# Performance work log

Hardware: AMD Instinct MI355X
Metric: run time of the kernel (lower is better)

The kernel has to match this reference:

```python
import jax, jax.numpy as jnp
import numpy as np

B, T, I, H, C = 4096, 512, 3, 32, 3  # batch, seq_len, input, hidden, classes


def setup_inputs() -> dict:
    key = jax.random.key(0)
    ks = jax.random.split(key, 7)
    s = 1.0 / np.sqrt(H)  # PyTorch LSTM init scale
    return {
        "x": jax.random.normal(ks[0], (B, T, I), dtype=jnp.float32),
        "W_ih": jax.random.normal(ks[1], (4 * H, I), dtype=jnp.float32) * s,
        "W_hh": jax.random.normal(ks[2], (4 * H, H), dtype=jnp.float32) * s,
        "b_ih": jax.random.normal(ks[3], (4 * H,), dtype=jnp.float32) * s,
        "b_hh": jax.random.normal(ks[4], (4 * H,), dtype=jnp.float32) * s,
        "W_fc": jax.random.normal(ks[5], (C, H), dtype=jnp.float32) * s,
        "b_fc": jax.random.normal(ks[6], (C,), dtype=jnp.float32) * s,
    }


def reference(x, W_ih, W_hh, b_ih, b_hh, W_fc, b_fc):
    # Precompute input contribution to all gates for every timestep: (B,T,4H)
    xg = jnp.einsum("bti,gi->btg", x, W_ih) + b_ih + b_hh
    h0 = jnp.zeros((x.shape[0], H), dtype=x.dtype)
    c0 = jnp.zeros_like(h0)

    def step(carry, xt):
        h, c = carry
        g = xt + h @ W_hh.T  # (B,4H)
        i_g, f_g, g_g, o_g = jnp.split(g, 4, axis=-1)  # PyTorch gate order i,f,g,o
        i_g = jax.nn.sigmoid(i_g)
        f_g = jax.nn.sigmoid(f_g)
        g_g = jnp.tanh(g_g)
        o_g = jax.nn.sigmoid(o_g)
        c = f_g * c + i_g * g_g
        h = o_g * jnp.tanh(c)
        return (h, c), None

    (h_last, _), _ = jax.lax.scan(step, (h0, c0), jnp.swapaxes(xg, 0, 1))
    return h_last @ W_fc.T + b_fc  # (B, num_classes)
```

## Files before the change

kernel.cpp:

```cpp
#include <hip/hip_runtime.h>
#include <cstdint>

#define B_TOT 4096
#define T_LEN 512
#define CHUNK 256
#define LOG2E 1.44269504088896340736f
#define HSTR  40

typedef _Float16 f16x8 __attribute__((ext_vector_type(8)));
typedef _Float16 f16x4 __attribute__((ext_vector_type(4)));
typedef float    f32x4 __attribute__((ext_vector_type(4)));

__device__ __forceinline__ float ex2(float v)  { return __builtin_amdgcn_exp2f(v); }
__device__ __forceinline__ float rcp_(float v) { return __builtin_amdgcn_rcpf(v); }

__global__ __launch_bounds__(256, 2)
void lstm_pr(const float* __restrict__ x,
             const float* __restrict__ W_ih,
             const float* __restrict__ W_hh,
             const float* __restrict__ b_ih,
             const float* __restrict__ b_hh,
             const float* __restrict__ W_fc,
             const float* __restrict__ b_fc,
             float* __restrict__ out)
{
    __shared__ __align__(16) _Float16 hbuf[2][8][HSTR];
    __shared__ __align__(16) _Float16 xbuf[CHUNK / 2][8][8];

    const int tid  = threadIdx.x;
    const int wave = tid >> 6;
    const int lane = tid & 63;
    const int n    = lane & 15;
    const int kq   = lane >> 4;
    const int nb   = n & 7;
    const int tb   = blockIdx.x * 8;

    const int   gate_m = n & 3;
    const int   hl_m   = n >> 2;
    const int   R1     = gate_m * 32 + 8 * wave + hl_m;
    const int   R2     = R1 + 4;
    const float sm     = (gate_m == 2) ? (-2.0f * LOG2E) : (-LOG2E);

    f16x8 aW1, aW2;
#pragma unroll
    for (int j = 0; j < 8; ++j) {
        aW1[j] = (_Float16)(sm * W_hh[R1 * 32 + 8 * kq + j]);
        aW2[j] = (_Float16)(sm * W_hh[R2 * 32 + 8 * kq + j]);
    }
    f16x8 a21 = {}, a22 = {};
    if (kq == 0) {
        a21[0] = (_Float16)(sm * W_ih[R1 * 3 + 0]);
        a21[1] = (_Float16)(sm * W_ih[R1 * 3 + 1]);
        a21[2] = (_Float16)(sm * W_ih[R1 * 3 + 2]);
        a21[3] = (_Float16)(sm * (b_ih[R1] + b_hh[R1]));
        a22[0] = (_Float16)(sm * W_ih[R2 * 3 + 0]);
        a22[1] = (_Float16)(sm * W_ih[R2 * 3 + 1]);
        a22[2] = (_Float16)(sm * W_ih[R2 * 3 + 2]);
        a22[3] = (_Float16)(sm * (b_ih[R2] + b_hh[R2]));
    }

    const int hid_s = 8 * wave + kq + ((n >> 3) ? 4 : 0);

    if (tid < 160) ((int*)&hbuf[0][0][0])[tid] = 0;

    const float K2 = -2.0f * LOG2E;
    float c = 0.0f;
    const f32x4 z = {0.f, 0.f, 0.f, 0.f};
    f32x4 accx1, accx2;

    const bool hi = (n >> 3) != 0;

    for (int tc = 0; tc < T_LEN; tc += CHUNK) {
#pragma unroll
        for (int s = 0; s < 8; ++s) {
            const int idx = tid + s * 256;
            const int tl = idx >> 3, m = idx & 7;
            const float* xp = x + ((size_t)(tb + m) * T_LEN + (tc + tl)) * 3;
            f16x4 v;
            v[0] = (_Float16)xp[0]; v[1] = (_Float16)xp[1];
            v[2] = (_Float16)xp[2]; v[3] = (_Float16)1.0f;
            *(f16x4*)&xbuf[tl >> 1][m][4 * (tl & 1)] = v;
        }
        __syncthreads();

        f16x8 xp = *(const f16x8*)&xbuf[0][nb][0];
        {
            const f16x8 b2 = __builtin_shufflevector(xp, xp, 0, 1, 2, 3, 0, 1, 2, 3);
            accx1 = __builtin_amdgcn_mfma_f32_16x16x32_f16(a21, b2, z, 0, 0, 0);
            accx2 = __builtin_amdgcn_mfma_f32_16x16x32_f16(a22, b2, z, 0, 0, 0);
        }

        for (int t2 = 0; t2 < CHUNK / 2; ++t2) {
            {
                const f16x8 bh = *(const f16x8*)&hbuf[0][nb][8 * kq];
                const f32x4 ac1 = __builtin_amdgcn_mfma_f32_16x16x32_f16(aW1, bh, accx1, 0, 0, 0);
                const f32x4 ac2 = __builtin_amdgcn_mfma_f32_16x16x32_f16(aW2, bh, accx2, 0, 0, 0);

                const float a0 = hi ? ac2[0] : ac1[0];
                const float a1 = hi ? ac2[1] : ac1[1];
                const float a2 = hi ? ac2[2] : ac1[2];
                const float a3 = hi ? ac2[3] : ac1[3];

                const float ei = ex2(a0), ef = ex2(a1), eg = ex2(a2), eo = ex2(a3);
                const float pi = 1.0f + ei, pf = 1.0f + ef, pg = 1.0f + eg;
                const float mg = 1.0f - eg;
                const float pp = pi * pg, qn = mg * pf;
                c = fmaf(c, pp, qn) * rcp_(pf * pp);
                const float ec = ex2(c * K2);
                const float po = 1.0f + eo, pc = 1.0f + ec, mc = 1.0f - ec;
                const float h = mc * rcp_(po * pc);
                hbuf[1][nb][hid_s] = (_Float16)h;

                const f16x8 b2 = __builtin_shufflevector(xp, xp, 4, 5, 6, 7, 4, 5, 6, 7);
                accx1 = __builtin_amdgcn_mfma_f32_16x16x32_f16(a21, b2, z, 0, 0, 0);
                accx2 = __builtin_amdgcn_mfma_f32_16x16x32_f16(a22, b2, z, 0, 0, 0);
            }
            __syncthreads();

            {
                const f16x8 bh = *(const f16x8*)&hbuf[1][nb][8 * kq];
                const int t2n = (t2 + 1) & (CHUNK / 2 - 1);
                const f16x8 xpN = *(const f16x8*)&xbuf[t2n][nb][0];

                const f32x4 ac1 = __builtin_amdgcn_mfma_f32_16x16x32_f16(aW1, bh, accx1, 0, 0, 0);
                const f32x4 ac2 = __builtin_amdgcn_mfma_f32_16x16x32_f16(aW2, bh, accx2, 0, 0, 0);

                const float a0 = hi ? ac2[0] : ac1[0];
                const float a1 = hi ? ac2[1] : ac1[1];
                const float a2 = hi ? ac2[2] : ac1[2];
                const float a3 = hi ? ac2[3] : ac1[3];

                const float ei = ex2(a0), ef = ex2(a1), eg = ex2(a2), eo = ex2(a3);
                const float pi = 1.0f + ei, pf = 1.0f + ef, pg = 1.0f + eg;
                const float mg = 1.0f - eg;
                const float pp = pi * pg, qn = mg * pf;
                c = fmaf(c, pp, qn) * rcp_(pf * pp);
                const float ec = ex2(c * K2);
                const float po = 1.0f + eo, pc = 1.0f + ec, mc = 1.0f - ec;
                const float h = mc * rcp_(po * pc);
                hbuf[0][nb][hid_s] = (_Float16)h;

                const f16x8 b2 = __builtin_shufflevector(xpN, xpN, 0, 1, 2, 3, 0, 1, 2, 3);
                accx1 = __builtin_amdgcn_mfma_f32_16x16x32_f16(a21, b2, z, 0, 0, 0);
                accx2 = __builtin_amdgcn_mfma_f32_16x16x32_f16(a22, b2, z, 0, 0, 0);
                xp = xpN;
            }
            __syncthreads();
        }
    }

    if (tid < 24) {
        const int m = tid / 3, cc = tid % 3;
        float acc = b_fc[cc];
#pragma unroll
        for (int k = 0; k < 32; ++k)
            acc = fmaf(W_fc[cc * 32 + k], (float)hbuf[0][m][k], acc);
        out[(tb + m) * 3 + cc] = acc;
    }
}

extern "C" void kernel_launch(void* const* d_in, const int* in_sizes, int n_in,
                              void* d_out, int out_size, void* d_ws, size_t ws_size,
                              hipStream_t stream) {
    const float* x    = (const float*)d_in[0];
    const float* W_ih = (const float*)d_in[1];
    const float* W_hh = (const float*)d_in[2];
    const float* b_ih = (const float*)d_in[3];
    const float* b_hh = (const float*)d_in[4];
    const float* W_fc = (const float*)d_in[5];
    const float* b_fc = (const float*)d_in[6];
    float* out = (float*)d_out;

    dim3 grid(B_TOT / 8);
    dim3 block(256);
    lstm_pr<<<grid, block, 0, stream>>>(x, W_ih, W_hh, b_ih, b_hh, W_fc, b_fc, out);
}
```

Baseline: 184.6 us.

## Run each LSTM recurrence in a single wavefront with swizzle-based hidden-state exchange

Restructures the kernel so one 64-lane wavefront handles 4 sequences and all 128 gate rows using 8 MFMAs per step, instead of 4 waves splitting the gates for 8 sequences. The hidden state is exchanged between lanes with ds_swizzle rather than an LDS buffer guarded by __syncthreads each timestep, removing block barriers from the serial recurrence. The whole sequence's inputs are staged into LDS up front. In exchange each wave does roughly twice the MFMA work per sequence, holds many more weight registers, and the grid has 1024 single-wave blocks, which changes occupancy and latency hiding.

New measurement: 244.1 us. +32.2%, slower.

```diff
diff --git a/kernel.cpp b/kernel.cpp
--- a/kernel.cpp
+++ b/kernel.cpp
@@ -3,19 +3,19 @@
 
 #define B_TOT 4096
 #define T_LEN 512
-#define CHUNK 256
 #define LOG2E 1.44269504088896340736f
-#define HSTR  40
 
 typedef _Float16 f16x8 __attribute__((ext_vector_type(8)));
 typedef _Float16 f16x4 __attribute__((ext_vector_type(4)));
+typedef _Float16 f16x2 __attribute__((ext_vector_type(2)));
 typedef float    f32x4 __attribute__((ext_vector_type(4)));
+typedef unsigned int u32x4 __attribute__((ext_vector_type(4)));
 
 __device__ __forceinline__ float ex2(float v)  { return __builtin_amdgcn_exp2f(v); }
 __device__ __forceinline__ float rcp_(float v) { return __builtin_amdgcn_rcpf(v); }
 
-__global__ __launch_bounds__(256, 2)
-void lstm_pr(const float* __restrict__ x,
+__global__ __launch_bounds__(64, 1)
+void lstm_wv(const float* __restrict__ x,
              const float* __restrict__ W_ih,
              const float* __restrict__ W_hh,
              const float* __restrict__ b_ih,
@@ -24,138 +24,122 @@
              const float* __restrict__ b_fc,
              float* __restrict__ out)
 {
-    __shared__ __align__(16) _Float16 hbuf[2][8][HSTR];
-    __shared__ __align__(16) _Float16 xbuf[CHUNK / 2][8][8];
+    __shared__ __align__(16) _Float16 xbuf[T_LEN / 2][4][8];
+    __shared__ float hfin[4][32];
 
-    const int tid  = threadIdx.x;
-    const int wave = tid >> 6;
-    const int lane = tid & 63;
+    const int lane = threadIdx.x;
     const int n    = lane & 15;
     const int kq   = lane >> 4;
-    const int nb   = n & 7;
-    const int tb   = blockIdx.x * 8;
+    const int b    = n & 3;
+    const int d    = n >> 2;
+    const int gb0  = blockIdx.x << 2;
 
-    const int   gate_m = n & 3;
-    const int   hl_m   = n >> 2;
-    const int   R1     = gate_m * 32 + 8 * wave + hl_m;
-    const int   R2     = R1 + 4;
-    const float sm     = (gate_m == 2) ? (-2.0f * LOG2E) : (-LOG2E);
-
-    f16x8 aW1, aW2;
+    f16x8 aW[8], A2e[8], A2o[8];
 #pragma unroll
     for (int j = 0; j < 8; ++j) {
-        aW1[j] = (_Float16)(sm * W_hh[R1 * 32 + 8 * kq + j]);
-        aW2[j] = (_Float16)(sm * W_hh[R2 * 32 + 8 * kq + j]);
-    }
-    f16x8 a21 = {}, a22 = {};
-    if (kq == 0) {
-        a21[0] = (_Float16)(sm * W_ih[R1 * 3 + 0]);
-        a21[1] = (_Float16)(sm * W_ih[R1 * 3 + 1]);
-        a21[2] = (_Float16)(sm * W_ih[R1 * 3 + 2]);
-        a21[3] = (_Float16)(sm * (b_ih[R1] + b_hh[R1]));
-        a22[0] = (_Float16)(sm * W_ih[R2 * 3 + 0]);
-        a22[1] = (_Float16)(sm * W_ih[R2 * 3 + 1]);
-        a22[2] = (_Float16)(sm * W_ih[R2 * 3 + 2]);
-        a22[3] = (_Float16)(sm * (b_ih[R2] + b_hh[R2]));
+        const int   g   = j & 3;
+        const int   R   = 32 * g + 8 * d + 4 * (j >> 2) + b;
+        const float smj = (g == 2) ? (-2.0f * LOG2E) : (-LOG2E);
+#pragma unroll
+        for (int jj = 0; jj < 8; ++jj)
+            aW[j][jj] = (_Float16)(smj * W_hh[R * 32 + 8 * kq + jj]);
+        f16x8 e = {}, o = {};
+        if (kq == 0) {
+            const _Float16 w0 = (_Float16)(smj * W_ih[R * 3 + 0]);
+            const _Float16 w1 = (_Float16)(smj * W_ih[R * 3 + 1]);
+            const _Float16 w2 = (_Float16)(smj * W_ih[R * 3 + 2]);
+            const _Float16 wb = (_Float16)(smj * (b_ih[R] + b_hh[R]));
+            e[0] = w0; e[1] = w1; e[2] = w2; e[3] = wb;
+            o[4] = w0; o[5] = w1; o[6] = w2; o[7] = wb;
+        }
+        A2e[j] = e; A2o[j] = o;
     }
 
-    const int hid_s = 8 * wave + kq + ((n >> 3) ? 4 : 0);
+    for (int s = 0; s < 32; ++s) {
+        const int id = lane + (s << 6);
+        const int t = id >> 2, bb = id & 3;
+        const float* xg = x + ((size_t)(gb0 + bb) * T_LEN + t) * 3;
+        f16x4 v;
+        v[0] = (_Float16)xg[0]; v[1] = (_Float16)xg[1];
+        v[2] = (_Float16)xg[2]; v[3] = (_Float16)1.0f;
+        *(f16x4*)&xbuf[t >> 1][bb][(t & 1) << 2] = v;
+    }
+    __syncthreads();
 
-    if (tid < 160) ((int*)&hbuf[0][0][0])[tid] = 0;
+    const bool selj = (d >= 2);
+    const bool selr = (d & 1) != 0;
+    const f32x4 z = {0.f, 0.f, 0.f, 0.f};
 
-    const float K2 = -2.0f * LOG2E;
-    float c = 0.0f;
-    const f32x4 z = {0.f, 0.f, 0.f, 0.f};
-    f32x4 accx1, accx2;
+    u32x4 bhu = {0u, 0u, 0u, 0u};
+    float c0 = 0.f, c1 = 0.f;
+    float h0 = 0.f, h1 = 0.f;
 
-    const bool hi = (n >> 3) != 0;
+    f16x8 xp = *(const f16x8*)&xbuf[0][b][0];
 
-    for (int tc = 0; tc < T_LEN; tc += CHUNK) {
+    for (int t2 = 0; t2 < T_LEN / 2; ++t2) {
+        const f16x8 xpN = *(const f16x8*)&xbuf[(t2 + 1) & (T_LEN / 2 - 1)][b][0];
 #pragma unroll
-        for (int s = 0; s < 8; ++s) {
-            const int idx = tid + s * 256;
-            const int tl = idx >> 3, m = idx & 7;
-            const float* xp = x + ((size_t)(tb + m) * T_LEN + (tc + tl)) * 3;
-            f16x4 v;
-            v[0] = (_Float16)xp[0]; v[1] = (_Float16)xp[1];
-            v[2] = (_Float16)xp[2]; v[3] = (_Float16)1.0f;
-            *(f16x4*)&xbuf[tl >> 1][m][4 * (tl & 1)] = v;
+        for (int par = 0; par < 2; ++par) {
+            f32x4 acc[8];
+#pragma unroll
+            for (int j = 0; j < 8; ++j) {
+                const f32x4 ax = __builtin_amdgcn_mfma_f32_16x16x32_f16(
+                    par ? A2o[j] : A2e[j], xp, z, 0, 0, 0);
+                acc[j] = __builtin_amdgcn_mfma_f32_16x16x32_f16(
+                    aW[j], __builtin_bit_cast(f16x8, bhu), ax, 0, 0, 0);
+            }
+            float av[4][2];
+#pragma unroll
+            for (int g = 0; g < 4; ++g) {
+                const float v0 = selj ? acc[g + 4][0] : acc[g][0];
+                const float v1 = selj ? acc[g + 4][1] : acc[g][1];
+                const float v2 = selj ? acc[g + 4][2] : acc[g][2];
+                const float v3 = selj ? acc[g + 4][3] : acc[g][3];
+                av[g][0] = selr ? v2 : v0;
+                av[g][1] = selr ? v3 : v1;
+            }
+            {
+                const float ei = ex2(av[0][0]), ef = ex2(av[1][0]);
+                const float eg = ex2(av[2][0]), eo = ex2(av[3][0]);
+                const float pi = 1.f + ei, pf = 1.f + ef, pg = 1.f + eg;
+                const float mg = 1.f - eg;
+                const float pp = pi * pg, qn = mg * pf;
+                c0 = fmaf(c0, pp, qn) * rcp_(pf * pp);
+                const float ec = ex2(c0 * (-2.0f * LOG2E));
+                const float po = 1.f + eo, pc = 1.f + ec, mc = 1.f - ec;
+                h0 = mc * rcp_(po * pc);
+            }
+            {
+                const float ei = ex2(av[0][1]), ef = ex2(av[1][1]);
+                const float eg = ex2(av[2][1]), eo = ex2(av[3][1]);
+                const float pi = 1.f + ei, pf = 1.f + ef, pg = 1.f + eg;
+                const float mg = 1.f - eg;
+                const float pp = pi * pg, qn = mg * pf;
+                c1 = fmaf(c1, pp, qn) * rcp_(pf * pp);
+                const float ec = ex2(c1 * (-2.0f * LOG2E));
+                const float po = 1.f + eo, pc = 1.f + ec, mc = 1.f - ec;
+                h1 = mc * rcp_(po * pc);
+            }
+            f16x2 hp; hp[0] = (_Float16)h0; hp[1] = (_Float16)h1;
+            const int pk = __builtin_bit_cast(int, hp);
+            bhu[0] = (unsigned)__builtin_amdgcn_ds_swizzle(pk, 0x0013);
+            bhu[1] = (unsigned)__builtin_amdgcn_ds_swizzle(pk, 0x0093);
+            bhu[2] = (unsigned)__builtin_amdgcn_ds_swizzle(pk, 0x0113);
+            bhu[3] = (unsigned)__builtin_amdgcn_ds_swizzle(pk, 0x0193);
         }
-        __syncthreads();
-
-        f16x8 xp = *(const f16x8*)&xbuf[0][nb][0];
-        {
-            const f16x8 b2 = __builtin_shufflevector(xp, xp, 0, 1, 2, 3, 0, 1, 2, 3);
-            accx1 = __builtin_amdgcn_mfma_f32_16x16x32_f16(a21, b2, z, 0, 0, 0);
-            accx2 = __builtin_amdgcn_mfma_f32_16x16x32_f16(a22, b2, z, 0, 0, 0);
-        }
-
-        for (int t2 = 0; t2 < CHUNK / 2; ++t2) {
-            {
-                const f16x8 bh = *(const f16x8*)&hbuf[0][nb][8 * kq];
-                const f32x4 ac1 = __builtin_amdgcn_mfma_f32_16x16x32_f16(aW1, bh, accx1, 0, 0, 0);
-                const f32x4 ac2 = __builtin_amdgcn_mfma_f32_16x16x32_f16(aW2, bh, accx2, 0, 0, 0);
-
-                const float a0 = hi ? ac2[0] : ac1[0];
-                const float a1 = hi ? ac2[1] : ac1[1];
-                const float a2 = hi ? ac2[2] : ac1[2];
-                const float a3 = hi ? ac2[3] : ac1[3];
-
-                const float ei = ex2(a0), ef = ex2(a1), eg = ex2(a2), eo = ex2(a3);
-                const float pi = 1.0f + ei, pf = 1.0f + ef, pg = 1.0f + eg;
-                const float mg = 1.0f - eg;
-                const float pp = pi * pg, qn = mg * pf;
-                c = fmaf(c, pp, qn) * rcp_(pf * pp);
-                const float ec = ex2(c * K2);
-                const float po = 1.0f + eo, pc = 1.0f + ec, mc = 1.0f - ec;
-                const float h = mc * rcp_(po * pc);
-                hbuf[1][nb][hid_s] = (_Float16)h;
-
-                const f16x8 b2 = __builtin_shufflevector(xp, xp, 4, 5, 6, 7, 4, 5, 6, 7);
-                accx1 = __builtin_amdgcn_mfma_f32_16x16x32_f16(a21, b2, z, 0, 0, 0);
-                accx2 = __builtin_amdgcn_mfma_f32_16x16x32_f16(a22, b2, z, 0, 0, 0);
-            }
-            __syncthreads();
-
-            {
-                const f16x8 bh = *(const f16x8*)&hbuf[1][nb][8 * kq];
-                const int t2n = (t2 + 1) & (CHUNK / 2 - 1);
-                const f16x8 xpN = *(const f16x8*)&xbuf[t2n][nb][0];
-
-                const f32x4 ac1 = __builtin_amdgcn_mfma_f32_16x16x32_f16(aW1, bh, accx1, 0, 0, 0);
-                const f32x4 ac2 = __builtin_amdgcn_mfma_f32_16x16x32_f16(aW2, bh, accx2, 0, 0, 0);
-
-                const float a0 = hi ? ac2[0] : ac1[0];
-                const float a1 = hi ? ac2[1] : ac1[1];
-                const float a2 = hi ? ac2[2] : ac1[2];
-                const float a3 = hi ? ac2[3] : ac1[3];
-
-                const float ei = ex2(a0), ef = ex2(a1), eg = ex2(a2), eo = ex2(a3);
-                const float pi = 1.0f + ei, pf = 1.0f + ef, pg = 1.0f + eg;
-                const float mg = 1.0f - eg;
-                const float pp = pi * pg, qn = mg * pf;
-                c = fmaf(c, pp, qn) * rcp_(pf * pp);
-                const float ec = ex2(c * K2);
-                const float po = 1.0f + eo, pc = 1.0f + ec, mc = 1.0f - ec;
-                const float h = mc * rcp_(po * pc);
-                hbuf[0][nb][hid_s] = (_Float16)h;
-
-                const f16x8 b2 = __builtin_shufflevector(xpN, xpN, 0, 1, 2, 3, 0, 1, 2, 3);
-                accx1 = __builtin_amdgcn_mfma_f32_16x16x32_f16(a21, b2, z, 0, 0, 0);
-                accx2 = __builtin_amdgcn_mfma_f32_16x16x32_f16(a22, b2, z, 0, 0, 0);
-                xp = xpN;
-            }
-            __syncthreads();
-        }
+        xp = xpN;
     }
 
-    if (tid < 24) {
-        const int m = tid / 3, cc = tid % 3;
+    hfin[b][8 * kq + 2 * d + 0] = h0;
+    hfin[b][8 * kq + 2 * d + 1] = h1;
+    __syncthreads();
+    if (lane < 12) {
+        const int m = lane / 3, cc = lane - 3 * m;
         float acc = b_fc[cc];
 #pragma unroll
         for (int k = 0; k < 32; ++k)
-            acc = fmaf(W_fc[cc * 32 + k], (float)hbuf[0][m][k], acc);
-        out[(tb + m) * 3 + cc] = acc;
+            acc = fmaf(W_fc[cc * 32 + k], hfin[m][k], acc);
+        out[(gb0 + m) * 3 + cc] = acc;
     }
 }
 
@@ -171,7 +155,7 @@
     const float* b_fc = (const float*)d_in[6];
     float* out = (float*)d_out;
 
-    dim3 grid(B_TOT / 8);
-    dim3 block(256);
-    lstm_pr<<<grid, block, 0, stream>>>(x, W_ih, W_hh, b_ih, b_hh, W_fc, b_fc, out);
+    dim3 grid(B_TOT / 4);
+    dim3 block(64);
+    lstm_wv<<<grid, block, 0, stream>>>(x, W_ih, W_hh, b_ih, b_hh, W_fc, b_fc, out);
 }
```

## Interleave two independent batch tiles per block to hide recurrence latency

Applied to the files above, without the earlier changes.

Each block now processes 16 sequences as two independent 8-sequence groups (A and B) whose timesteps alternate. The hbuf buffers are repurposed so each group's h-state lives in its own slot, and the next group's h is prefetched into registers across the barrier. The aim is to overlap one group's MFMA and transcendental latency with the other's, keeping the serial chain per barrier shorter in effective cost. Blocks are halved in number, occupancy hint drops to 1, and CHUNK is halved to fit the larger x staging buffer. This risks fewer resident waves per CU and more barriers per real timestep.

Result: slower. 252.8 us (+36.9%).

```diff
diff --git a/kernel.cpp b/kernel.cpp
--- a/kernel.cpp
+++ b/kernel.cpp
@@ -3,7 +3,7 @@
 
 #define B_TOT 4096
 #define T_LEN 512
-#define CHUNK 256
+#define CHUNK 128
 #define LOG2E 1.44269504088896340736f
 #define HSTR  40
 
@@ -14,8 +14,8 @@
 __device__ __forceinline__ float ex2(float v)  { return __builtin_amdgcn_exp2f(v); }
 __device__ __forceinline__ float rcp_(float v) { return __builtin_amdgcn_rcpf(v); }
 
-__global__ __launch_bounds__(256, 2)
-void lstm_pr(const float* __restrict__ x,
+__global__ __launch_bounds__(256, 1)
+void lstm_2t(const float* __restrict__ x,
              const float* __restrict__ W_ih,
              const float* __restrict__ W_hh,
              const float* __restrict__ b_ih,
@@ -25,7 +25,7 @@
              float* __restrict__ out)
 {
     __shared__ __align__(16) _Float16 hbuf[2][8][HSTR];
-    __shared__ __align__(16) _Float16 xbuf[CHUNK / 2][8][8];
+    __shared__ __align__(16) _Float16 xbuf[CHUNK / 2][16][8];
 
     const int tid  = threadIdx.x;
     const int wave = tid >> 6;
@@ -33,7 +33,7 @@
     const int n    = lane & 15;
     const int kq   = lane >> 4;
     const int nb   = n & 7;
-    const int tb   = blockIdx.x * 8;
+    const int tb   = blockIdx.x * 16;
 
     const int   gate_m = n & 3;
     const int   hl_m   = n >> 2;
@@ -60,101 +60,143 @@
     }
 
     const int hid_s = 8 * wave + kq + ((n >> 3) ? 4 : 0);
-
-    if (tid < 160) ((int*)&hbuf[0][0][0])[tid] = 0;
+    const bool hi   = (n >> 3) != 0;
+
+    for (int i = tid; i < 320; i += 256) ((int*)&hbuf[0][0][0])[i] = 0;
 
     const float K2 = -2.0f * LOG2E;
-    float c = 0.0f;
+    float cA = 0.0f, cB = 0.0f;
     const f32x4 z = {0.f, 0.f, 0.f, 0.f};
-    f32x4 accx1, accx2;
-
-    const bool hi = (n >> 3) != 0;
+    f32x4 accA1, accA2, accB1, accB2;
+    f16x8 bhA = {}, bhB = {};
 
     for (int tc = 0; tc < T_LEN; tc += CHUNK) {
 #pragma unroll
         for (int s = 0; s < 8; ++s) {
             const int idx = tid + s * 256;
-            const int tl = idx >> 3, m = idx & 7;
-            const float* xp = x + ((size_t)(tb + m) * T_LEN + (tc + tl)) * 3;
+            const int tl = idx >> 4, m = idx & 15;
+            const float* xp_ = x + ((size_t)(tb + m) * T_LEN + (tc + tl)) * 3;
             f16x4 v;
-            v[0] = (_Float16)xp[0]; v[1] = (_Float16)xp[1];
-            v[2] = (_Float16)xp[2]; v[3] = (_Float16)1.0f;
+            v[0] = (_Float16)xp_[0]; v[1] = (_Float16)xp_[1];
+            v[2] = (_Float16)xp_[2]; v[3] = (_Float16)1.0f;
             *(f16x4*)&xbuf[tl >> 1][m][4 * (tl & 1)] = v;
         }
         __syncthreads();
 
-        f16x8 xp = *(const f16x8*)&xbuf[0][nb][0];
+        f16x8 xpA = *(const f16x8*)&xbuf[0][nb][0];
+        f16x8 xpB = *(const f16x8*)&xbuf[0][8 + nb][0];
         {
-            const f16x8 b2 = __builtin_shufflevector(xp, xp, 0, 1, 2, 3, 0, 1, 2, 3);
-            accx1 = __builtin_amdgcn_mfma_f32_16x16x32_f16(a21, b2, z, 0, 0, 0);
-            accx2 = __builtin_amdgcn_mfma_f32_16x16x32_f16(a22, b2, z, 0, 0, 0);
+            const f16x8 bA = __builtin_shufflevector(xpA, xpA, 0, 1, 2, 3, 0, 1, 2, 3);
+            accA1 = __builtin_amdgcn_mfma_f32_16x16x32_f16(a21, bA, z, 0, 0, 0);
+            accA2 = __builtin_amdgcn_mfma_f32_16x16x32_f16(a22, bA, z, 0, 0, 0);
+            const f16x8 bB = __builtin_shufflevector(xpB, xpB, 0, 1, 2, 3, 0, 1, 2, 3);
+            accB1 = __builtin_amdgcn_mfma_f32_16x16x32_f16(a21, bB, z, 0, 0, 0);
+            accB2 = __builtin_amdgcn_mfma_f32_16x16x32_f16(a22, bB, z, 0, 0, 0);
         }
 
         for (int t2 = 0; t2 < CHUNK / 2; ++t2) {
-            {
-                const f16x8 bh = *(const f16x8*)&hbuf[0][nb][8 * kq];
-                const f32x4 ac1 = __builtin_amdgcn_mfma_f32_16x16x32_f16(aW1, bh, accx1, 0, 0, 0);
-                const f32x4 ac2 = __builtin_amdgcn_mfma_f32_16x16x32_f16(aW2, bh, accx2, 0, 0, 0);
-
-                const float a0 = hi ? ac2[0] : ac1[0];
-                const float a1 = hi ? ac2[1] : ac1[1];
-                const float a2 = hi ? ac2[2] : ac1[2];
-                const float a3 = hi ? ac2[3] : ac1[3];
-
-                const float ei = ex2(a0), ef = ex2(a1), eg = ex2(a2), eo = ex2(a3);
-                const float pi = 1.0f + ei, pf = 1.0f + ef, pg = 1.0f + eg;
-                const float mg = 1.0f - eg;
-                const float pp = pi * pg, qn = mg * pf;
-                c = fmaf(c, pp, qn) * rcp_(pf * pp);
-                const float ec = ex2(c * K2);
-                const float po = 1.0f + eo, pc = 1.0f + ec, mc = 1.0f - ec;
-                const float h = mc * rcp_(po * pc);
-                hbuf[1][nb][hid_s] = (_Float16)h;
-
-                const f16x8 b2 = __builtin_shufflevector(xp, xp, 4, 5, 6, 7, 4, 5, 6, 7);
-                accx1 = __builtin_amdgcn_mfma_f32_16x16x32_f16(a21, b2, z, 0, 0, 0);
-                accx2 = __builtin_amdgcn_mfma_f32_16x16x32_f16(a22, b2, z, 0, 0, 0);
-            }
-            __syncthreads();
-
-            {
-                const f16x8 bh = *(const f16x8*)&hbuf[1][nb][8 * kq];
-                const int t2n = (t2 + 1) & (CHUNK / 2 - 1);
+            const int t2n = (t2 + 1) & (CHUNK / 2 - 1);
+
+            {
+                const f16x8 pf = *(const f16x8*)&hbuf[1][nb][8 * kq];
+                const f32x4 ac1 = __builtin_amdgcn_mfma_f32_16x16x32_f16(aW1, bhA, accA1, 0, 0, 0);
+                const f32x4 ac2 = __builtin_amdgcn_mfma_f32_16x16x32_f16(aW2, bhA, accA2, 0, 0, 0);
+                const float a0 = hi ? ac2[0] : ac1[0];
+                const float a1 = hi ? ac2[1] : ac1[1];
+                const float a2 = hi ? ac2[2] : ac1[2];
+                const float a3 = hi ? ac2[3] : ac1[3];
+                const float ei = ex2(a0), ef = ex2(a1), eg = ex2(a2), eo = ex2(a3);
+                const float pi = 1.0f + ei, pfd = 1.0f + ef, pg = 1.0f + eg;
+                const float mg = 1.0f - eg;
+                const float pp = pi * pg, qn = mg * pfd;
+                cA = fmaf(cA, pp, qn) * rcp_(pfd * pp);
+                const float ec = ex2(cA * K2);
+                const float po = 1.0f + eo, pc = 1.0f + ec, mc = 1.0f - ec;
+                hbuf[0][nb][hid_s] = (_Float16)(mc * rcp_(po * pc));
+                const f16x8 b2 = __builtin_shufflevector(xpA, xpA, 4, 5, 6, 7, 4, 5, 6, 7);
+                accA1 = __builtin_amdgcn_mfma_f32_16x16x32_f16(a21, b2, z, 0, 0, 0);
+                accA2 = __builtin_amdgcn_mfma_f32_16x16x32_f16(a22, b2, z, 0, 0, 0);
+                bhB = pf;
+            }
+            __syncthreads();
+            {
+                const f16x8 pf = *(const f16x8*)&hbuf[0][nb][8 * kq];
+                const f32x4 ac1 = __builtin_amdgcn_mfma_f32_16x16x32_f16(aW1, bhB, accB1, 0, 0, 0);
+                const f32x4 ac2 = __builtin_amdgcn_mfma_f32_16x16x32_f16(aW2, bhB, accB2, 0, 0, 0);
+                const float a0 = hi ? ac2[0] : ac1[0];
+                const float a1 = hi ? ac2[1] : ac1[1];
+                const float a2 = hi ? ac2[2] : ac1[2];
+                const float a3 = hi ? ac2[3] : ac1[3];
+                const float ei = ex2(a0), ef = ex2(a1), eg = ex2(a2), eo = ex2(a3);
+                const float pi = 1.0f + ei, pfd = 1.0f + ef, pg = 1.0f + eg;
+                const float mg = 1.0f - eg;
+                const float pp = pi * pg, qn = mg * pfd;
+                cB = fmaf(cB, pp, qn) * rcp_(pfd * pp);
+                const float ec = ex2(cB * K2);
+                const float po = 1.0f + eo, pc = 1.0f + ec, mc = 1.0f - ec;
+                hbuf[1][nb][hid_s] = (_Float16)(mc * rcp_(po * pc));
+                const f16x8 b2 = __builtin_shufflevector(xpB, xpB, 4, 5, 6, 7, 4, 5, 6, 7);
+                accB1 = __builtin_amdgcn_mfma_f32_16x16x32_f16(a21, b2, z, 0, 0, 0);
+                accB2 = __builtin_amdgcn_mfma_f32_16x16x32_f16(a22, b2, z, 0, 0, 0);
+                bhA = pf;
+            }
+            __syncthreads();
+
+            {
+                const f16x8 pf  = *(const f16x8*)&hbuf[1][nb][8 * kq];
                 const f16x8 xpN = *(const f16x8*)&xbuf[t2n][nb][0];
-
-                const f32x4 ac1 = __builtin_amdgcn_mfma_f32_16x16x32_f16(aW1, bh, accx1, 0, 0, 0);
-                const f32x4 ac2 = __builtin_amdgcn_mfma_f32_16x16x32_f16(aW2, bh, accx2, 0, 0, 0);
-
-                const float a0 = hi ? ac2[0] : ac1[0];
-                const float a1 = hi ? ac2[1] : ac1[1];
-                const float a2 = hi ? ac2[2] : ac1[2];
-                const float a3 = hi ? ac2[3] : ac1[3];
-
-                const float ei = ex2(a0), ef = ex2(a1), eg = ex2(a2), eo = ex2(a3);
-                const float pi = 1.0f + ei, pf = 1.0f + ef, pg = 1.0f + eg;
-                const float mg = 1.0f - eg;
-                const float pp = pi * pg, qn = mg * pf;
-                c = fmaf(c, pp, qn) * rcp_(pf * pp);
-                const float ec = ex2(c * K2);
-                const float po = 1.0f + eo, pc = 1.0f + ec, mc = 1.0f - ec;
-                const float h = mc * rcp_(po * pc);
-                hbuf[0][nb][hid_s] = (_Float16)h;
-
+                const f32x4 ac1 = __builtin_amdgcn_mfma_f32_16x16x32_f16(aW1, bhA, accA1, 0, 0, 0);
+                const f32x4 ac2 = __builtin_amdgcn_mfma_f32_16x16x32_f16(aW2, bhA, accA2, 0, 0, 0);
+                const float a0 = hi ? ac2[0] : ac1[0];
+                const float a1 = hi ? ac2[1] : ac1[1];
+                const float a2 = hi ? ac2[2] : ac1[2];
+                const float a3 = hi ? ac2[3] : ac1[3];
+                const float ei = ex2(a0), ef = ex2(a1), eg = ex2(a2), eo = ex2(a3);
+                const float pi = 1.0f + ei, pfd = 1.0f + ef, pg = 1.0f + eg;
+                const float mg = 1.0f - eg;
+                const float pp = pi * pg, qn = mg * pfd;
+                cA = fmaf(cA, pp, qn) * rcp_(pfd * pp);
+                const float ec = ex2(cA * K2);
+                const float po = 1.0f + eo, pc = 1.0f + ec, mc = 1.0f - ec;
+                hbuf[0][nb][hid_s] = (_Float16)(mc * rcp_(po * pc));
                 const f16x8 b2 = __builtin_shufflevector(xpN, xpN, 0, 1, 2, 3, 0, 1, 2, 3);
-                accx1 = __builtin_amdgcn_mfma_f32_16x16x32_f16(a21, b2, z, 0, 0, 0);
-                accx2 = __builtin_amdgcn_mfma_f32_16x16x32_f16(a22, b2, z, 0, 0, 0);
-                xp = xpN;
+                accA1 = __builtin_amdgcn_mfma_f32_16x16x32_f16(a21, b2, z, 0, 0, 0);
+                accA2 = __builtin_amdgcn_mfma_f32_16x16x32_f16(a22, b2, z, 0, 0, 0);
+                bhB = pf; xpA = xpN;
+            }
+            __syncthreads();
+            {
+                const f16x8 pf  = *(const f16x8*)&hbuf[0][nb][8 * kq];
+                const f16x8 xpN = *(const f16x8*)&xbuf[t2n][8 + nb][0];
+                const f32x4 ac1 = __builtin_amdgcn_mfma_f32_16x16x32_f16(aW1, bhB, accB1, 0, 0, 0);
+                const f32x4 ac2 = __builtin_amdgcn_mfma_f32_16x16x32_f16(aW2, bhB, accB2, 0, 0, 0);
+                const float a0 = hi ? ac2[0] : ac1[0];
+                const float a1 = hi ? ac2[1] : ac1[1];
+                const float a2 = hi ? ac2[2] : ac1[2];
+                const float a3 = hi ? ac2[3] : ac1[3];
+                const float ei = ex2(a0), ef = ex2(a1), eg = ex2(a2), eo = ex2(a3);
+                const float pi = 1.0f + ei, pfd = 1.0f + ef, pg = 1.0f + eg;
+                const float mg = 1.0f - eg;
+                const float pp = pi * pg, qn = mg * pfd;
+                cB = fmaf(cB, pp, qn) * rcp_(pfd * pp);
+                const float ec = ex2(cB * K2);
+                const float po = 1.0f + eo, pc = 1.0f + ec, mc = 1.0f - ec;
+                hbuf[1][nb][hid_s] = (_Float16)(mc * rcp_(po * pc));
+                const f16x8 b2 = __builtin_shufflevector(xpN, xpN, 0, 1, 2, 3, 0, 1, 2, 3);
+                accB1 = __builtin_amdgcn_mfma_f32_16x16x32_f16(a21, b2, z, 0, 0, 0);
+                accB2 = __builtin_amdgcn_mfma_f32_16x16x32_f16(a22, b2, z, 0, 0, 0);
+                bhA = pf; xpB = xpN;
             }
             __syncthreads();
         }
     }
 
-    if (tid < 24) {
-        const int m = tid / 3, cc = tid % 3;
+    if (tid < 48) {
+        const int m = tid / 3, cc = tid - 3 * (tid / 3);
         float acc = b_fc[cc];
 #pragma unroll
         for (int k = 0; k < 32; ++k)
-            acc = fmaf(W_fc[cc * 32 + k], (float)hbuf[0][m][k], acc);
+            acc = fmaf(W_fc[cc * 32 + k], (float)hbuf[m >> 3][m & 7][k], acc);
         out[(tb + m) * 3 + cc] = acc;
     }
 }
@@ -171,7 +213,7 @@
     const float* b_fc = (const float*)d_in[6];
     float* out = (float*)d_out;
 
-    dim3 grid(B_TOT / 8);
+    dim3 grid(B_TOT / 16);
     dim3 block(256);
-    lstm_pr<<<grid, block, 0, stream>>>(x, W_ih, W_hh, b_ih, b_hh, W_fc, b_fc, out);
+    lstm_2t<<<grid, block, 0, stream>>>(x, W_ih, W_hh, b_ih, b_hh, W_fc, b_fc, out);
 }
```

## Interleave two independent batch groups per block to hide recurrence latency

Applied to the files above, without the earlier changes.

Each block now handles 16 batch rows as two independent 8-row groups. Their MFMA and gate computations are interleaved within each timestep, so one group's latency-bound recurrence can overlap the other's. The grid is halved and the launch bound changed to one block per CU hint, and the x staging buffer and h buffers double. This adds register pressure and may reduce the number of resident blocks, trading parallelism across blocks for ILP within each block.

After: 240.0 us. 1.3x slower.

```diff
diff --git a/kernel.cpp b/kernel.cpp
--- a/kernel.cpp
+++ b/kernel.cpp
@@ -14,8 +14,8 @@
 __device__ __forceinline__ float ex2(float v)  { return __builtin_amdgcn_exp2f(v); }
 __device__ __forceinline__ float rcp_(float v) { return __builtin_amdgcn_rcpf(v); }
 
-__global__ __launch_bounds__(256, 2)
-void lstm_pr(const float* __restrict__ x,
+__global__ __launch_bounds__(256, 1)
+void lstm_il(const float* __restrict__ x,
              const float* __restrict__ W_ih,
              const float* __restrict__ W_hh,
              const float* __restrict__ b_ih,
@@ -24,8 +24,8 @@
              const float* __restrict__ b_fc,
              float* __restrict__ out)
 {
-    __shared__ __align__(16) _Float16 hbuf[2][8][HSTR];
-    __shared__ __align__(16) _Float16 xbuf[CHUNK / 2][8][8];
+    __shared__ __align__(16) _Float16 hbuf[2][2][8][HSTR];
+    __shared__ __align__(16) _Float16 xbuf[CHUNK / 2][16][8];
 
     const int tid  = threadIdx.x;
     const int wave = tid >> 6;
@@ -33,7 +33,7 @@
     const int n    = lane & 15;
     const int kq   = lane >> 4;
     const int nb   = n & 7;
-    const int tb   = blockIdx.x * 8;
+    const int tb   = blockIdx.x * 16;
 
     const int   gate_m = n & 3;
     const int   hl_m   = n >> 2;
@@ -60,101 +60,139 @@
     }
 
     const int hid_s = 8 * wave + kq + ((n >> 3) ? 4 : 0);
-
-    if (tid < 160) ((int*)&hbuf[0][0][0])[tid] = 0;
+    const bool hi   = (n >> 3) != 0;
+
+    for (int i = tid; i < 640; i += 256) ((int*)&hbuf[0][0][0][0])[i] = 0;
 
     const float K2 = -2.0f * LOG2E;
-    float c = 0.0f;
+    float cA = 0.0f, cB = 0.0f;
     const f32x4 z = {0.f, 0.f, 0.f, 0.f};
-    f32x4 accx1, accx2;
-
-    const bool hi = (n >> 3) != 0;
+    f32x4 accA1, accA2, accB1, accB2;
 
     for (int tc = 0; tc < T_LEN; tc += CHUNK) {
 #pragma unroll
-        for (int s = 0; s < 8; ++s) {
+        for (int s = 0; s < 16; ++s) {
             const int idx = tid + s * 256;
-            const int tl = idx >> 3, m = idx & 7;
-            const float* xp = x + ((size_t)(tb + m) * T_LEN + (tc + tl)) * 3;
+            const int tl = idx >> 4, m = idx & 15;
+            const float* xp_ = x + ((size_t)(tb + m) * T_LEN + (tc + tl)) * 3;
             f16x4 v;
-            v[0] = (_Float16)xp[0]; v[1] = (_Float16)xp[1];
-            v[2] = (_Float16)xp[2]; v[3] = (_Float16)1.0f;
+            v[0] = (_Float16)xp_[0]; v[1] = (_Float16)xp_[1];
+            v[2] = (_Float16)xp_[2]; v[3] = (_Float16)1.0f;
             *(f16x4*)&xbuf[tl >> 1][m][4 * (tl & 1)] = v;
         }
         __syncthreads();
 
-        f16x8 xp = *(const f16x8*)&xbuf[0][nb][0];
+        f16x8 xpA = *(const f16x8*)&xbuf[0][nb][0];
+        f16x8 xpB = *(const f16x8*)&xbuf[0][8 + nb][0];
         {
-            const f16x8 b2 = __builtin_shufflevector(xp, xp, 0, 1, 2, 3, 0, 1, 2, 3);
-            accx1 = __builtin_amdgcn_mfma_f32_16x16x32_f16(a21, b2, z, 0, 0, 0);
-            accx2 = __builtin_amdgcn_mfma_f32_16x16x32_f16(a22, b2, z, 0, 0, 0);
+            const f16x8 bA = __builtin_shufflevector(xpA, xpA, 0, 1, 2, 3, 0, 1, 2, 3);
+            accA1 = __builtin_amdgcn_mfma_f32_16x16x32_f16(a21, bA, z, 0, 0, 0);
+            accA2 = __builtin_amdgcn_mfma_f32_16x16x32_f16(a22, bA, z, 0, 0, 0);
+            const f16x8 bB = __builtin_shufflevector(xpB, xpB, 0, 1, 2, 3, 0, 1, 2, 3);
+            accB1 = __builtin_amdgcn_mfma_f32_16x16x32_f16(a21, bB, z, 0, 0, 0);
+            accB2 = __builtin_amdgcn_mfma_f32_16x16x32_f16(a22, bB, z, 0, 0, 0);
         }
 
         for (int t2 = 0; t2 < CHUNK / 2; ++t2) {
+            const int t2n = (t2 + 1) & (CHUNK / 2 - 1);
+
             {
-                const f16x8 bh = *(const f16x8*)&hbuf[0][nb][8 * kq];
-                const f32x4 ac1 = __builtin_amdgcn_mfma_f32_16x16x32_f16(aW1, bh, accx1, 0, 0, 0);
-                const f32x4 ac2 = __builtin_amdgcn_mfma_f32_16x16x32_f16(aW2, bh, accx2, 0, 0, 0);
-
-                const float a0 = hi ? ac2[0] : ac1[0];
-                const float a1 = hi ? ac2[1] : ac1[1];
-                const float a2 = hi ? ac2[2] : ac1[2];
-                const float a3 = hi ? ac2[3] : ac1[3];
-
-                const float ei = ex2(a0), ef = ex2(a1), eg = ex2(a2), eo = ex2(a3);
-                const float pi = 1.0f + ei, pf = 1.0f + ef, pg = 1.0f + eg;
-                const float mg = 1.0f - eg;
-                const float pp = pi * pg, qn = mg * pf;
-                c = fmaf(c, pp, qn) * rcp_(pf * pp);
-                const float ec = ex2(c * K2);
-                const float po = 1.0f + eo, pc = 1.0f + ec, mc = 1.0f - ec;
-                const float h = mc * rcp_(po * pc);
-                hbuf[1][nb][hid_s] = (_Float16)h;
-
-                const f16x8 b2 = __builtin_shufflevector(xp, xp, 4, 5, 6, 7, 4, 5, 6, 7);
-                accx1 = __builtin_amdgcn_mfma_f32_16x16x32_f16(a21, b2, z, 0, 0, 0);
-                accx2 = __builtin_amdgcn_mfma_f32_16x16x32_f16(a22, b2, z, 0, 0, 0);
+                const f16x8 bhA = *(const f16x8*)&hbuf[0][0][nb][8 * kq];
+                const f16x8 bhB = *(const f16x8*)&hbuf[1][0][nb][8 * kq];
+                const f32x4 aA1 = __builtin_amdgcn_mfma_f32_16x16x32_f16(aW1, bhA, accA1, 0, 0, 0);
+                const f32x4 aA2 = __builtin_amdgcn_mfma_f32_16x16x32_f16(aW2, bhA, accA2, 0, 0, 0);
+                const f32x4 aB1 = __builtin_amdgcn_mfma_f32_16x16x32_f16(aW1, bhB, accB1, 0, 0, 0);
+                const f32x4 aB2 = __builtin_amdgcn_mfma_f32_16x16x32_f16(aW2, bhB, accB2, 0, 0, 0);
+
+                const float xA0 = hi ? aA2[0] : aA1[0];
+                const float xA1 = hi ? aA2[1] : aA1[1];
+                const float xA2 = hi ? aA2[2] : aA1[2];
+                const float xA3 = hi ? aA2[3] : aA1[3];
+                const float eiA = ex2(xA0), efA = ex2(xA1), egA = ex2(xA2), eoA = ex2(xA3);
+                const float piA = 1.f + eiA, pfA = 1.f + efA, pgA = 1.f + egA;
+                const float mgA = 1.f - egA;
+                const float ppA = piA * pgA, qnA = mgA * pfA;
+                cA = fmaf(cA, ppA, qnA) * rcp_(pfA * ppA);
+                const float ecA = ex2(cA * K2);
+                const float poA = 1.f + eoA, pcA = 1.f + ecA, mcA = 1.f - ecA;
+                hbuf[0][1][nb][hid_s] = (_Float16)(mcA * rcp_(poA * pcA));
+
+                const float xB0 = hi ? aB2[0] : aB1[0];
+                const float xB1 = hi ? aB2[1] : aB1[1];
+                const float xB2 = hi ? aB2[2] : aB1[2];
+                const float xB3 = hi ? aB2[3] : aB1[3];
+                const float eiB = ex2(xB0), efB = ex2(xB1), egB = ex2(xB2), eoB = ex2(xB3);
+                const float piB = 1.f + eiB, pfB = 1.f + efB, pgB = 1.f + egB;
+                const float mgB = 1.f - egB;
+                const float ppB = piB * pgB, qnB = mgB * pfB;
+                cB = fmaf(cB, ppB, qnB) * rcp_(pfB * ppB);
+                const float ecB = ex2(cB * K2);
+                const float poB = 1.f + eoB, pcB = 1.f + ecB, mcB = 1.f - ecB;
+                hbuf[1][1][nb][hid_s] = (_Float16)(mcB * rcp_(poB * pcB));
+
+                const f16x8 b2A = __builtin_shufflevector(xpA, xpA, 4, 5, 6, 7, 4, 5, 6, 7);
+                accA1 = __builtin_amdgcn_mfma_f32_16x16x32_f16(a21, b2A, z, 0, 0, 0);
+                accA2 = __builtin_amdgcn_mfma_f32_16x16x32_f16(a22, b2A, z, 0, 0, 0);
+                const f16x8 b2B = __builtin_shufflevector(xpB, xpB, 4, 5, 6, 7, 4, 5, 6, 7);
+                accB1 = __builtin_amdgcn_mfma_f32_16x16x32_f16(a21, b2B, z, 0, 0, 0);
+                accB2 = __builtin_amdgcn_mfma_f32_16x16x32_f16(a22, b2B, z, 0, 0, 0);
             }
             __syncthreads();
 
             {
-                const f16x8 bh = *(const f16x8*)&hbuf[1][nb][8 * kq];
-                const int t2n = (t2 + 1) & (CHUNK / 2 - 1);
-                const f16x8 xpN = *(const f16x8*)&xbuf[t2n][nb][0];
-
-                const f32x4 ac1 = __builtin_amdgcn_mfma_f32_16x16x32_f16(aW1, bh, accx1, 0, 0, 0);
-                const f32x4 ac2 = __builtin_amdgcn_mfma_f32_16x16x32_f16(aW2, bh, accx2, 0, 0, 0);
-
-                const float a0 = hi ? ac2[0] : ac1[0];
-                const float a1 = hi ? ac2[1] : ac1[1];
-                const float a2 = hi ? ac2[2] : ac1[2];
-                const float a3 = hi ? ac2[3] : ac1[3];
-
-                const float ei = ex2(a0), ef = ex2(a1), eg = ex2(a2), eo = ex2(a3);
-                const float pi = 1.0f + ei, pf = 1.0f + ef, pg = 1.0f + eg;
-                const float mg = 1.0f - eg;
-                const float pp = pi * pg, qn = mg * pf;
-                c = fmaf(c, pp, qn) * rcp_(pf * pp);
-                const float ec = ex2(c * K2);
-                const float po = 1.0f + eo, pc = 1.0f + ec, mc = 1.0f - ec;
-                const float h = mc * rcp_(po * pc);
-                hbuf[0][nb][hid_s] = (_Float16)h;
-
-                const f16x8 b2 = __builtin_shufflevector(xpN, xpN, 0, 1, 2, 3, 0, 1, 2, 3);
-                accx1 = __builtin_amdgcn_mfma_f32_16x16x32_f16(a21, b2, z, 0, 0, 0);
-                accx2 = __builtin_amdgcn_mfma_f32_16x16x32_f16(a22, b2, z, 0, 0, 0);
-                xp = xpN;
+                const f16x8 bhA = *(const f16x8*)&hbuf[0][1][nb][8 * kq];
+                const f16x8 bhB = *(const f16x8*)&hbuf[1][1][nb][8 * kq];
+                const f16x8 xpAN = *(const f16x8*)&xbuf[t2n][nb][0];
+                const f16x8 xpBN = *(const f16x8*)&xbuf[t2n][8 + nb][0];
+                const f32x4 aA1 = __builtin_amdgcn_mfma_f32_16x16x32_f16(aW1, bhA, accA1, 0, 0, 0);
+                const f32x4 aA2 = __builtin_amdgcn_mfma_f32_16x16x32_f16(aW2, bhA, accA2, 0, 0, 0);
+                const f32x4 aB1 = __builtin_amdgcn_mfma_f32_16x16x32_f16(aW1, bhB, accB1, 0, 0, 0);
+                const f32x4 aB2 = __builtin_amdgcn_mfma_f32_16x16x32_f16(aW2, bhB, accB2, 0, 0, 0);
+
+                const float xA0 = hi ? aA2[0] : aA1[0];
+                const float xA1 = hi ? aA2[1] : aA1[1];
+                const float xA2 = hi ? aA2[2] : aA1[2];
+                const float xA3 = hi ? aA2[3] : aA1[3];
+                const float eiA = ex2(xA0), efA = ex2(xA1), egA = ex2(xA2), eoA = ex2(xA3);
+                const float piA = 1.f + eiA, pfA = 1.f + efA, pgA = 1.f + egA;
+                const float mgA = 1.f - egA;
+                const float ppA = piA * pgA, qnA = mgA * pfA;
+                cA = fmaf(cA, ppA, qnA) * rcp_(pfA * ppA);
+                const float ecA = ex2(cA * K2);
+                const float poA = 1.f + eoA, pcA = 1.f + ecA, mcA = 1.f - ecA;
+                hbuf[0][0][nb][hid_s] = (_Float16)(mcA * rcp_(poA * pcA));
+
+                const float xB0 = hi ? aB2[0] : aB1[0];
+                const float xB1 = hi ? aB2[1] : aB1[1];
+                const float xB2 = hi ? aB2[2] : aB1[2];
+                const float xB3 = hi ? aB2[3] : aB1[3];
+                const float eiB = ex2(xB0), efB = ex2(xB1), egB = ex2(xB2), eoB = ex2(xB3);
+                const float piB = 1.f + eiB, pfB = 1.f + efB, pgB = 1.f + egB;
+                const float mgB = 1.f - egB;
+                const float ppB = piB * pgB, qnB = mgB * pfB;
+                cB = fmaf(cB, ppB, qnB) * rcp_(pfB * ppB);
+                const float ecB = ex2(cB * K2);
+                const float poB = 1.f + eoB, pcB = 1.f + ecB, mcB = 1.f - ecB;
+                hbuf[1][0][nb][hid_s] = (_Float16)(mcB * rcp_(poB * pcB));
+
+                const f16x8 b2A = __builtin_shufflevector(xpAN, xpAN, 0, 1, 2, 3, 0, 1, 2, 3);
+                accA1 = __builtin_amdgcn_mfma_f32_16x16x32_f16(a21, b2A, z, 0, 0, 0);
+                accA2 = __builtin_amdgcn_mfma_f32_16x16x32_f16(a22, b2A, z, 0, 0, 0);
+                const f16x8 b2B = __builtin_shufflevector(xpBN, xpBN, 0, 1, 2, 3, 0, 1, 2, 3);
+                accB1 = __builtin_amdgcn_mfma_f32_16x16x32_f16(a21, b2B, z, 0, 0, 0);
+                accB2 = __builtin_amdgcn_mfma_f32_16x16x32_f16(a22, b2B, z, 0, 0, 0);
+                xpA = xpAN; xpB = xpBN;
             }
             __syncthreads();
         }
     }
 
-    if (tid < 24) {
-        const int m = tid / 3, cc = tid % 3;
+    if (tid < 48) {
+        const int m = tid / 3, cc = tid - 3 * (tid / 3);
         float acc = b_fc[cc];
 #pragma unroll
         for (int k = 0; k < 32; ++k)
-            acc = fmaf(W_fc[cc * 32 + k], (float)hbuf[0][m][k], acc);
+            acc = fmaf(W_fc[cc * 32 + k], (float)hbuf[m >> 3][0][m & 7][k], acc);
         out[(tb + m) * 3 + cc] = acc;
     }
 }
@@ -171,7 +209,7 @@
     const float* b_fc = (const float*)d_in[6];
     float* out = (float*)d_out;
 
-    dim3 grid(B_TOT / 8);
+    dim3 grid(B_TOT / 16);
     dim3 block(256);
-    lstm_pr<<<grid, block, 0, stream>>>(x, W_ih, W_hh, b_ih, b_hh, W_fc, b_fc, out);
+    lstm_il<<<grid, block, 0, stream>>>(x, W_ih, W_hh, b_ih, b_hh, W_fc, b_fc, out);
 }
```
